# Performance work log

Hardware: AMD Instinct MI355X
Metric: run time of the kernel (lower is better)

## Reference

```python
import jax, jax.numpy as jnp
import numpy as np

D_MODEL = 1024
NUM_HEADS = 16
D_K = D_MODEL // NUM_HEADS


def setup_inputs() -> dict:
    key = jax.random.key(0)
    ks = jax.random.split(key, 7)
    B, S = 4, 2048
    scale = 1.0 / np.sqrt(D_MODEL)
    return {
        "query": jax.random.normal(ks[0], (B, S, D_MODEL), dtype=jnp.float32),
        "key": jax.random.normal(ks[1], (B, S, D_MODEL), dtype=jnp.float32),
        "value": jax.random.normal(ks[2], (B, S, D_MODEL), dtype=jnp.float32),
        "W_q": jax.random.normal(ks[3], (D_MODEL, D_MODEL), dtype=jnp.float32) * scale,
        "W_k": jax.random.normal(ks[4], (D_MODEL, D_MODEL), dtype=jnp.float32) * scale,
        "W_v": jax.random.normal(ks[5], (D_MODEL, D_MODEL), dtype=jnp.float32) * scale,
        "W_o": jax.random.normal(ks[6], (D_MODEL, D_MODEL), dtype=jnp.float32) * scale,
    }


def reference(query, key, value, W_q, W_k, W_v, W_o):
    B, S, _ = query.shape
    # nn.Linear applies x @ W.T; project then split heads: (B, H, S, d_k)
    def proj(x, W):
        return (x @ W.T).reshape(B, S, NUM_HEADS, D_K).transpose(0, 2, 1, 3)
    Q = proj(query, W_q)
    K = proj(key, W_k)
    V = proj(value, W_v)
    # naive full-score attention: (B, H, S, S)
    scores = jnp.einsum("bhqd,bhkd->bhqk", Q, K) / jnp.sqrt(jnp.float32(D_K))
    attn = jax.nn.softmax(scores, axis=-1)
    out = jnp.einsum("bhqk,bhkd->bhqd", attn, V)  # (B, H, S, d_k)
    out = out.transpose(0, 2, 1, 3).reshape(B, S, D_MODEL)
    return out @ W_o.T
```

## Files before the change

kernel.cpp:

```cpp
#include <hip/hip_runtime.h>
#include <hip/hip_bf16.h>
#include <cstdint>
#include <cstddef>

static constexpr int S  = 2048;
static constexpr int DM = 1024;
static constexpr int NH = 16;
static constexpr int BB = 4;
static constexpr int MR = BB * S;

typedef __bf16 bf16x8 __attribute__((ext_vector_type(8)));
typedef float  f32x4  __attribute__((ext_vector_type(4)));
typedef float  f32x16 __attribute__((ext_vector_type(16)));
typedef unsigned int uint2v __attribute__((ext_vector_type(2)));

__device__ __forceinline__ f32x4 mfma16(bf16x8 a, bf16x8 b, f32x4 c) {
    return __builtin_amdgcn_mfma_f32_16x16x32_bf16(a, b, c, 0, 0, 0);
}
__device__ __forceinline__ f32x16 mfma32(bf16x8 a, bf16x8 b, f32x16 c) {
    return __builtin_amdgcn_mfma_f32_32x32x16_bf16(a, b, c, 0, 0, 0);
}

__device__ __forceinline__ unsigned int cvt_pk_bf16(float lo, float hi) {
    unsigned int r;
    asm("v_cvt_pk_bf16_f32 %0, %1, %2" : "=v"(r) : "v"(lo), "v"(hi));
    return r;
}

struct CvtArgs {
    const float* src[7];
    __hip_bfloat16* dst[7];
    int n[7];
    float scl[7];
};

__global__ __launch_bounds__(256) void cvt_kernel(CvtArgs a) {
    const int t = blockIdx.y;
    const int i = (blockIdx.x * 256 + threadIdx.x) * 4;
    if (i >= a.n[t]) return;
    const float s = a.scl[t];
    const float4 v = *reinterpret_cast<const float4*>(a.src[t] + i);
    union { __hip_bfloat16 h[4]; short4 s4; } u;
    u.h[0] = __float2bfloat16(v.x * s);
    u.h[1] = __float2bfloat16(v.y * s);
    u.h[2] = __float2bfloat16(v.z * s);
    u.h[3] = __float2bfloat16(v.w * s);
    *reinterpret_cast<short4*>(a.dst[t] + i) = u.s4;
}

struct ProjArgs {
    const __hip_bfloat16* X[3];
    const __hip_bfloat16* W[3];
    __hip_bfloat16* O[3];
};

__global__ __launch_bounds__(256) void proj_kernel(ProjArgs a)
{
    __shared__ __align__(16) unsigned char smem[65536];
    __hip_bfloat16* Ts = reinterpret_cast<__hip_bfloat16*>(smem);

    const int id    = blockIdx.x;
    const int which = id >> 9;
    const int rem   = id & 511;
    const int xcd   = rem & 7, idx = rem >> 3;
    const int ystrip = xcd * 8 + (idx >> 3);
    const int xblk   = idx & 7;

    const __hip_bfloat16* __restrict__ X = a.X[which];
    const __hip_bfloat16* __restrict__ W = a.W[which];
    __hip_bfloat16* __restrict__ O = a.O[which];

    const int tid  = threadIdx.x;
    const int wave = tid >> 6, lane = tid & 63;
    const int wm = wave >> 1, wn = wave & 1;
    const int lr = lane & 15, lg = lane >> 4;
    const int m0 = ystrip * 128;
    const int n0 = xblk * 128;
    constexpr int K = DM;

    const int srow = tid >> 3, scol = (tid & 7) * 8;

    auto stage = [&](int bsel, int kt) {
        __hip_bfloat16* As = reinterpret_cast<__hip_bfloat16*>(smem + bsel * 32768);
        __hip_bfloat16* Bs = reinterpret_cast<__hip_bfloat16*>(smem + bsel * 32768 + 16384);
#pragma unroll
        for (int r = 0; r < 4; ++r) {
            const int c = r * 256 + tid;
            const int row = srow + r * 32;
            __builtin_amdgcn_global_load_lds(
                (const __attribute__((address_space(1))) void*)&X[(size_t)(m0 + row) * K + kt + scol],
                (__attribute__((address_space(3))) void*)&As[c * 8], 16, 0, 0);
            __builtin_amdgcn_global_load_lds(
                (const __attribute__((address_space(1))) void*)&W[(size_t)(n0 + row) * K + kt + scol],
                (__attribute__((address_space(3))) void*)&Bs[c * 8], 16, 0, 0);
        }
    };

    f32x4 acc[4][4] = {};

    stage(0, 0);
    int cur = 0;
    for (int kt = 0; kt < K; kt += 64) {
        __syncthreads();
        if (kt + 64 < K) stage(cur ^ 1, kt + 64);

        const __hip_bfloat16* As = reinterpret_cast<const __hip_bfloat16*>(smem + cur * 32768);
        const __hip_bfloat16* Bs = reinterpret_cast<const __hip_bfloat16*>(smem + cur * 32768 + 16384);
#pragma unroll
        for (int ks = 0; ks < 2; ++ks) {
            bf16x8 af[4], bfr[4];
#pragma unroll
            for (int i = 0; i < 4; ++i)
                af[i] = *reinterpret_cast<const bf16x8*>(&As[(wm * 64 + i * 16 + lr) * 64 + ks * 32 + lg * 8]);
#pragma unroll
            for (int i = 0; i < 4; ++i)
                bfr[i] = *reinterpret_cast<const bf16x8*>(&Bs[(wn * 64 + i * 16 + lr) * 64 + ks * 32 + lg * 8]);
#pragma unroll
            for (int mi = 0; mi < 4; ++mi)
#pragma unroll
                for (int ni = 0; ni < 4; ++ni)
                    acc[mi][ni] = mfma16(af[mi], bfr[ni], acc[mi][ni]);
        }
        cur ^= 1;
    }

    __syncthreads();
    if (which == 2) {
#pragma unroll
        for (int mi = 0; mi < 4; ++mi)
#pragma unroll
            for (int ni = 0; ni < 4; ++ni)
#pragma unroll
                for (int j = 0; j < 4; ++j) {
                    const int nl = wn * 64 + ni * 16 + lr;
                    const int ml = wm * 64 + mi * 16 + lg * 4 + j;
                    Ts[nl * 136 + ml] = __float2bfloat16(acc[mi][ni][j]);
                }
        __syncthreads();
        const int b = m0 >> 11, s0 = m0 & (S - 1);
#pragma unroll
        for (int r = 0; r < 8; ++r) {
            const int i2 = r * 256 + tid;
            const int nl = i2 >> 4, mc = i2 & 15;
            const uint4 val = *reinterpret_cast<const uint4*>(&Ts[nl * 136 + mc * 8]);
            const int h = (n0 + nl) >> 6, d = (n0 + nl) & 63;
            *reinterpret_cast<uint4*>(
                &O[(((size_t)b * NH + h) * 64 + d) * S + s0 + mc * 8]) = val;
        }
    } else {
#pragma unroll
        for (int mi = 0; mi < 4; ++mi)
#pragma unroll
            for (int ni = 0; ni < 4; ++ni)
#pragma unroll
                for (int j = 0; j < 4; ++j) {
                    const int ml = wm * 64 + mi * 16 + lg * 4 + j;
                    const int nl = wn * 64 + ni * 16 + lr;
                    Ts[ml * 136 + nl] = __float2bfloat16(acc[mi][ni][j]);
                }
        __syncthreads();
#pragma unroll
        for (int r = 0; r < 8; ++r) {
            const int i2 = r * 256 + tid;
            const int ml = i2 >> 4, mc = i2 & 15;
            const uint4 val = *reinterpret_cast<const uint4*>(&Ts[ml * 136 + mc * 8]);
            const int m = m0 + ml, n = n0 + mc * 8;
            const int b = m >> 11, s = m & (S - 1);
            const int h = n >> 6,  d = n & 63;
            *reinterpret_cast<uint4*>(
                &O[((((size_t)b * NH + h) * S + s) << 6) + d]) = val;
        }
    }
}

__global__ __launch_bounds__(256) void gemm_out(
    const __hip_bfloat16* __restrict__ X,
    const __hip_bfloat16* __restrict__ W,
    float* __restrict__ C, int M, int N, int K)
{
    __shared__ __align__(16) unsigned char smem[65536];

    const int id  = blockIdx.x;
    const int xcd = id & 7, idx = id >> 3;
    const int m0 = (xcd * 8 + (idx >> 3)) * 128;
    const int n0 = (idx & 7) * 128;

    const int tid  = threadIdx.x;
    const int wave = tid >> 6, lane = tid & 63;
    const int wm = wave >> 1, wn = wave & 1;
    const int lr = lane & 15, lg = lane >> 4;

    const int srow = tid >> 3, scol = (tid & 7) * 8;

    auto stage = [&](int bsel, int kt) {
        __hip_bfloat16* As = reinterpret_cast<__hip_bfloat16*>(smem + bsel * 32768);
        __hip_bfloat16* Bs = reinterpret_cast<__hip_bfloat16*>(smem + bsel * 32768 + 16384);
#pragma unroll
        for (int r = 0; r < 4; ++r) {
            const int c = r * 256 + tid;
            const int row = srow + r * 32;
            __builtin_amdgcn_global_load_lds(
                (const __attribute__((address_space(1))) void*)&X[(size_t)(m0 + row) * K + kt + scol],
                (__attribute__((address_space(3))) void*)&As[c * 8], 16, 0, 0);
            __builtin_amdgcn_global_load_lds(
                (const __attribute__((address_space(1))) void*)&W[(size_t)(n0 + row) * K + kt + scol],
                (__attribute__((address_space(3))) void*)&Bs[c * 8], 16, 0, 0);
        }
    };

    f32x4 acc[4][4] = {};

    stage(0, 0);
    int cur = 0;
    for (int kt = 0; kt < K; kt += 64) {
        __syncthreads();
        if (kt + 64 < K) stage(cur ^ 1, kt + 64);

        const __hip_bfloat16* As = reinterpret_cast<const __hip_bfloat16*>(smem + cur * 32768);
        const __hip_bfloat16* Bs = reinterpret_cast<const __hip_bfloat16*>(smem + cur * 32768 + 16384);
#pragma unroll
        for (int ks = 0; ks < 2; ++ks) {
            bf16x8 af[4], bfr[4];
#pragma unroll
            for (int i = 0; i < 4; ++i)
                af[i] = *reinterpret_cast<const bf16x8*>(&As[(wm * 64 + i * 16 + lr) * 64 + ks * 32 + lg * 8]);
#pragma unroll
            for (int i = 0; i < 4; ++i)
                bfr[i] = *reinterpret_cast<const bf16x8*>(&Bs[(wn * 64 + i * 16 + lr) * 64 + ks * 32 + lg * 8]);
#pragma unroll
            for (int mi = 0; mi < 4; ++mi)
#pragma unroll
                for (int ni = 0; ni < 4; ++ni)
                    acc[mi][ni] = mfma16(af[mi], bfr[ni], acc[mi][ni]);
        }
        cur ^= 1;
    }

#pragma unroll
    for (int mi = 0; mi < 4; ++mi)
#pragma unroll
        for (int ni = 0; ni < 4; ++ni)
#pragma unroll
            for (int j = 0; j < 4; ++j) {
                const int m = m0 + wm * 64 + mi * 16 + lg * 4 + j;
                const int n = n0 + wn * 64 + ni * 16 + lr;
                C[(size_t)m * N + n] = acc[mi][ni][j];
            }
}

__global__ __launch_bounds__(256) void attn_kernel(
    const __hip_bfloat16* __restrict__ Qp,
    const __hip_bfloat16* __restrict__ Kp,
    const __hip_bfloat16* __restrict__ VpT,
    __hip_bfloat16* __restrict__ Oc)
{
    constexpr int LP = 72;
    constexpr int NT = S / 64;
    __shared__ __hip_bfloat16 Ks[2][64][LP];
    __shared__ __hip_bfloat16 Vt[2][64][LP];

    const int tid  = threadIdx.x;
    const int wave = tid >> 6, lane = tid & 63;
    const int l31 = lane & 31, hi = lane >> 5;

    const int id  = blockIdx.x;
    const int xcd = id & 7, idx = id >> 3;
    const int bh   = xcd + 8 * (idx >> 4);
    const int qblk = idx & 15;

    const int b = bh >> 4, h = bh & (NH - 1);
    const int q0 = qblk * 128 + wave * 32;

    const __hip_bfloat16* Qh  = Qp  + (size_t)bh * S * 64;
    const __hip_bfloat16* Kh  = Kp  + (size_t)bh * S * 64;
    const __hip_bfloat16* VhT = VpT + (size_t)bh * S * 64;

    const int srow0 = tid >> 3,         scol = (tid & 7) * 8;
    const int srow1 = (256 + tid) >> 3;

    bf16x8 qf[4];
#pragma unroll
    for (int ds = 0; ds < 4; ++ds)
        qf[ds] = *reinterpret_cast<const bf16x8*>(
            &Qh[(size_t)(q0 + l31) * 64 + ds * 16 + hi * 8]);

    bf16x8 onesf;
#pragma unroll
    for (int i = 0; i < 8; ++i) onesf[i] = (__bf16)1.0f;

    f32x16 o[2] = {};
    f32x16 osum = {};
    const f32x16 zero16 = {};

    uint4 kreg0, kreg1, vreg0, vreg1;
    kreg0 = *reinterpret_cast<const uint4*>(&Kh[(size_t)srow0 * 64 + scol]);
    kreg1 = *reinterpret_cast<const uint4*>(&Kh[(size_t)srow1 * 64 + scol]);
    vreg0 = *reinterpret_cast<const uint4*>(&VhT[(size_t)srow0 * S + scol]);
    vreg1 = *reinterpret_cast<const uint4*>(&VhT[(size_t)srow1 * S + scol]);
    *reinterpret_cast<uint4*>(&Ks[0][srow0][scol]) = kreg0;
    *reinterpret_cast<uint4*>(&Ks[0][srow1][scol]) = kreg1;
    *reinterpret_cast<uint4*>(&Vt[0][srow0][scol]) = vreg0;
    *reinterpret_cast<uint4*>(&Vt[0][srow1][scol]) = vreg1;

    for (int t = 0; t < NT; ++t) {
        const int cur = t & 1;
        __syncthreads();

        if (t + 1 < NT) {
            const int kt = (t + 1) * 64;
            kreg0 = *reinterpret_cast<const uint4*>(&Kh[(size_t)(kt + srow0) * 64 + scol]);
            kreg1 = *reinterpret_cast<const uint4*>(&Kh[(size_t)(kt + srow1) * 64 + scol]);
            vreg0 = *reinterpret_cast<const uint4*>(&VhT[(size_t)srow0 * S + kt + scol]);
            vreg1 = *reinterpret_cast<const uint4*>(&VhT[(size_t)srow1 * S + kt + scol]);
        }

        f32x16 scf[2];
        __builtin_amdgcn_s_setprio(1);
        {
            bf16x8 kfr0 = *reinterpret_cast<const bf16x8*>(&Ks[cur][l31][hi * 8]);
            bf16x8 kfr1 = *reinterpret_cast<const bf16x8*>(&Ks[cur][32 + l31][hi * 8]);
            scf[0] = mfma32(kfr0, qf[0], zero16);
            scf[1] = mfma32(kfr1, qf[0], zero16);
        }
#pragma unroll
        for (int ds = 1; ds < 4; ++ds) {
            bf16x8 kfr0 = *reinterpret_cast<const bf16x8*>(&Ks[cur][l31][ds * 16 + hi * 8]);
            bf16x8 kfr1 = *reinterpret_cast<const bf16x8*>(&Ks[cur][32 + l31][ds * 16 + hi * 8]);
            scf[0] = mfma32(kfr0, qf[ds], scf[0]);
            scf[1] = mfma32(kfr1, qf[ds], scf[1]);
        }
        __builtin_amdgcn_s_setprio(0);

        unsigned int w[2][8];
#pragma unroll
        for (int kf = 0; kf < 2; ++kf)
#pragma unroll
            for (int t8 = 0; t8 < 8; ++t8)
                w[kf][t8] = cvt_pk_bf16(
                    __builtin_amdgcn_exp2f(scf[kf][2 * t8]),
                    __builtin_amdgcn_exp2f(scf[kf][2 * t8 + 1]));

        __builtin_amdgcn_s_setprio(1);
#pragma unroll
        for (int kb = 0; kb < 4; ++kb) {
            const int kf = kb >> 1, tb = (kb & 1) * 4;
            uint2v r02 = __builtin_amdgcn_permlane32_swap(w[kf][tb + 0], w[kf][tb + 2], false, false);
            uint2v r13 = __builtin_amdgcn_permlane32_swap(w[kf][tb + 1], w[kf][tb + 3], false, false);
            union { unsigned int u[4]; bf16x8 v; } pf;
            pf.u[0] = r02[0]; pf.u[1] = r13[0]; pf.u[2] = r02[1]; pf.u[3] = r13[1];
            bf16x8 vf0 = *reinterpret_cast<const bf16x8*>(&Vt[cur][l31][kb * 16 + hi * 8]);
            bf16x8 vf1 = *reinterpret_cast<const bf16x8*>(&Vt[cur][32 + l31][kb * 16 + hi * 8]);
            o[0] = mfma32(pf.v, vf0, o[0]);
            o[1] = mfma32(pf.v, vf1, o[1]);
            osum = mfma32(pf.v, onesf, osum);
        }
        __builtin_amdgcn_s_setprio(0);

        if (t + 1 < NT) {
            const int nxt = cur ^ 1;
            *reinterpret_cast<uint4*>(&Ks[nxt][srow0][scol]) = kreg0;
            *reinterpret_cast<uint4*>(&Ks[nxt][srow1][scol]) = kreg1;
            *reinterpret_cast<uint4*>(&Vt[nxt][srow0][scol]) = vreg0;
            *reinterpret_cast<uint4*>(&Vt[nxt][srow1][scol]) = vreg1;
        }
    }

    float inv[16];
#pragma unroll
    for (int r = 0; r < 16; ++r) inv[r] = 1.0f / osum[r];
#pragma unroll
    for (int df = 0; df < 2; ++df)
#pragma unroll
        for (int r = 0; r < 16; ++r) {
            const int qrow = (r & 3) + 8 * (r >> 2) + 4 * hi;
            const size_t row = (size_t)b * S + q0 + qrow;
            const int col = h * 64 + df * 32 + l31;
            Oc[row * DM + col] = __float2bfloat16(o[df][r] * inv[r]);
        }
}

extern "C" void kernel_launch(void* const* d_in, const int* in_sizes, int n_in,
                              void* d_out, int out_size, void* d_ws, size_t ws_size,
                              hipStream_t stream)
{
    const float* q  = (const float*)d_in[0];
    const float* k  = (const float*)d_in[1];
    const float* v  = (const float*)d_in[2];
    const float* wq = (const float*)d_in[3];
    const float* wk = (const float*)d_in[4];
    const float* wv = (const float*)d_in[5];
    const float* wo = (const float*)d_in[6];

    const size_t NE = (size_t)MR * DM;
    const size_t WE = (size_t)DM * DM;

    const size_t need = (7 * NE + 4 * WE) * sizeof(__hip_bfloat16);
    if (ws_size < need) return;

    __hip_bfloat16* p   = (__hip_bfloat16*)d_ws;
    __hip_bfloat16* qb  = p; p += NE;
    __hip_bfloat16* kb  = p; p += NE;
    __hip_bfloat16* vb  = p; p += NE;
    __hip_bfloat16* wqb = p; p += WE;
    __hip_bfloat16* wkb = p; p += WE;
    __hip_bfloat16* wvb = p; p += WE;
    __hip_bfloat16* wob = p; p += WE;
    __hip_bfloat16* Qp  = p; p += NE;
    __hip_bfloat16* Kp  = p; p += NE;
    __hip_bfloat16* VpT = p; p += NE;
    __hip_bfloat16* Oc  = p; p += NE;

    constexpr float SC = 0.18033688011112042f;

    CvtArgs ca;
    ca.src[0] = q;  ca.src[1] = k;  ca.src[2] = v;
    ca.src[3] = wq; ca.src[4] = wk; ca.src[5] = wv; ca.src[6] = wo;
    ca.dst[0] = qb;  ca.dst[1] = kb;  ca.dst[2] = vb;
    ca.dst[3] = wqb; ca.dst[4] = wkb; ca.dst[5] = wvb; ca.dst[6] = wob;
    for (int i = 0; i < 7; ++i) {
        ca.n[i] = (i < 3) ? (int)NE : (int)WE;
        ca.scl[i] = (i == 3) ? SC : 1.0f;
    }

    cvt_kernel<<<dim3((unsigned)(NE / 1024), 7), 256, 0, stream>>>(ca);

    ProjArgs pa;
    pa.X[0] = qb;  pa.X[1] = kb;  pa.X[2] = vb;
    pa.W[0] = wqb; pa.W[1] = wkb; pa.W[2] = wvb;
    pa.O[0] = Qp;  pa.O[1] = Kp;  pa.O[2] = VpT;

    proj_kernel<<<dim3(1536), 256, 0, stream>>>(pa);

    attn_kernel<<<dim3(1024), 256, 0, stream>>>(Qp, Kp, VpT, Oc);

    gemm_out<<<dim3(512), 256, 0, stream>>>(Oc, wob, (float*)d_out, MR, DM, DM);
}
```

Before: 207.2 us.

## Fuse fp32-to-bf16 activation conversion into projection GEMM A-tile loads

The projection kernel now reads fp32 query/key/value directly into registers, converts them to bf16 and writes them to LDS after the MFMA loop, prefetching the next tile. The standalone conversion pass over the three large activations is dropped, and the converter now handles only the four weight matrices. This removes a full read/write round trip of about 100MB of activation traffic and shrinks the workspace. The cost is twice the global read bytes per A tile inside the GEMM, plus extra registers and VALU conversion work that may reduce occupancy or overlap.

Result: no change. 210.6 us (+1.6%).

```diff
diff --git a/kernel.cpp b/kernel.cpp
--- a/kernel.cpp
+++ b/kernel.cpp
@@ -28,10 +28,10 @@
 }
 
 struct CvtArgs {
-    const float* src[7];
-    __hip_bfloat16* dst[7];
-    int n[7];
-    float scl[7];
+    const float* src[4];
+    __hip_bfloat16* dst[4];
+    int n[4];
+    float scl[4];
 };
 
 __global__ __launch_bounds__(256) void cvt_kernel(CvtArgs a) {
@@ -49,7 +49,7 @@
 }
 
 struct ProjArgs {
-    const __hip_bfloat16* X[3];
+    const float* X[3];
     const __hip_bfloat16* W[3];
     __hip_bfloat16* O[3];
 };
@@ -66,7 +66,7 @@
     const int ystrip = xcd * 8 + (idx >> 3);
     const int xblk   = idx & 7;
 
-    const __hip_bfloat16* __restrict__ X = a.X[which];
+    const float* __restrict__ X = a.X[which];
     const __hip_bfloat16* __restrict__ W = a.W[which];
     __hip_bfloat16* __restrict__ O = a.O[which];
 
@@ -80,29 +80,49 @@
 
     const int srow = tid >> 3, scol = (tid & 7) * 8;
 
-    auto stage = [&](int bsel, int kt) {
-        __hip_bfloat16* As = reinterpret_cast<__hip_bfloat16*>(smem + bsel * 32768);
+    float4 areg[8];
+
+    auto issue = [&](int bsel, int kt) {
         __hip_bfloat16* Bs = reinterpret_cast<__hip_bfloat16*>(smem + bsel * 32768 + 16384);
 #pragma unroll
         for (int r = 0; r < 4; ++r) {
             const int c = r * 256 + tid;
             const int row = srow + r * 32;
-            __builtin_amdgcn_global_load_lds(
-                (const __attribute__((address_space(1))) void*)&X[(size_t)(m0 + row) * K + kt + scol],
-                (__attribute__((address_space(3))) void*)&As[c * 8], 16, 0, 0);
+            const float* src = &X[(size_t)(m0 + row) * K + kt + scol];
+            areg[2 * r]     = *reinterpret_cast<const float4*>(src);
+            areg[2 * r + 1] = *reinterpret_cast<const float4*>(src + 4);
             __builtin_amdgcn_global_load_lds(
                 (const __attribute__((address_space(1))) void*)&W[(size_t)(n0 + row) * K + kt + scol],
                 (__attribute__((address_space(3))) void*)&Bs[c * 8], 16, 0, 0);
         }
     };
+    auto writeA = [&](int bsel) {
+        __hip_bfloat16* As = reinterpret_cast<__hip_bfloat16*>(smem + bsel * 32768);
+#pragma unroll
+        for (int r = 0; r < 4; ++r) {
+            const int c = r * 256 + tid;
+            union { __hip_bfloat16 h[8]; uint4 u4; } pk;
+            pk.h[0] = __float2bfloat16(areg[2 * r].x);
+            pk.h[1] = __float2bfloat16(areg[2 * r].y);
+            pk.h[2] = __float2bfloat16(areg[2 * r].z);
+            pk.h[3] = __float2bfloat16(areg[2 * r].w);
+            pk.h[4] = __float2bfloat16(areg[2 * r + 1].x);
+            pk.h[5] = __float2bfloat16(areg[2 * r + 1].y);
+            pk.h[6] = __float2bfloat16(areg[2 * r + 1].z);
+            pk.h[7] = __float2bfloat16(areg[2 * r + 1].w);
+            *reinterpret_cast<uint4*>(&As[c * 8]) = pk.u4;
+        }
+    };
 
     f32x4 acc[4][4] = {};
 
-    stage(0, 0);
+    issue(0, 0);
+    writeA(0);
     int cur = 0;
     for (int kt = 0; kt < K; kt += 64) {
         __syncthreads();
-        if (kt + 64 < K) stage(cur ^ 1, kt + 64);
+        const bool more = (kt + 64 < K);
+        if (more) issue(cur ^ 1, kt + 64);
 
         const __hip_bfloat16* As = reinterpret_cast<const __hip_bfloat16*>(smem + cur * 32768);
         const __hip_bfloat16* Bs = reinterpret_cast<const __hip_bfloat16*>(smem + cur * 32768 + 16384);
@@ -121,6 +141,7 @@
                 for (int ni = 0; ni < 4; ++ni)
                     acc[mi][ni] = mfma16(af[mi], bfr[ni], acc[mi][ni]);
         }
+        if (more) writeA(cur ^ 1);
         cur ^= 1;
     }
 
@@ -394,13 +415,10 @@
     const size_t NE = (size_t)MR * DM;
     const size_t WE = (size_t)DM * DM;
 
-    const size_t need = (7 * NE + 4 * WE) * sizeof(__hip_bfloat16);
+    const size_t need = (4 * NE + 4 * WE) * sizeof(__hip_bfloat16);
     if (ws_size < need) return;
 
     __hip_bfloat16* p   = (__hip_bfloat16*)d_ws;
-    __hip_bfloat16* qb  = p; p += NE;
-    __hip_bfloat16* kb  = p; p += NE;
-    __hip_bfloat16* vb  = p; p += NE;
     __hip_bfloat16* wqb = p; p += WE;
     __hip_bfloat16* wkb = p; p += WE;
     __hip_bfloat16* wvb = p; p += WE;
@@ -413,19 +431,17 @@
     constexpr float SC = 0.18033688011112042f;
 
     CvtArgs ca;
-    ca.src[0] = q;  ca.src[1] = k;  ca.src[2] = v;
-    ca.src[3] = wq; ca.src[4] = wk; ca.src[5] = wv; ca.src[6] = wo;
-    ca.dst[0] = qb;  ca.dst[1] = kb;  ca.dst[2] = vb;
-    ca.dst[3] = wqb; ca.dst[4] = wkb; ca.dst[5] = wvb; ca.dst[6] = wob;
-    for (int i = 0; i < 7; ++i) {
-        ca.n[i] = (i < 3) ? (int)NE : (int)WE;
-        ca.scl[i] = (i == 3) ? SC : 1.0f;
+    ca.src[0] = wq; ca.src[1] = wk; ca.src[2] = wv; ca.src[3] = wo;
+    ca.dst[0] = wqb; ca.dst[1] = wkb; ca.dst[2] = wvb; ca.dst[3] = wob;
+    for (int i = 0; i < 4; ++i) {
+        ca.n[i] = (int)WE;
+        ca.scl[i] = (i == 0) ? SC : 1.0f;
     }
 
-    cvt_kernel<<<dim3((unsigned)(NE / 1024), 7), 256, 0, stream>>>(ca);
+    cvt_kernel<<<dim3((unsigned)(WE / 1024), 4), 256, 0, stream>>>(ca);
 
     ProjArgs pa;
-    pa.X[0] = qb;  pa.X[1] = kb;  pa.X[2] = vb;
+    pa.X[0] = q;   pa.X[1] = k;   pa.X[2] = v;
     pa.W[0] = wqb; pa.W[1] = wkb; pa.W[2] = wvb;
     pa.O[0] = Qp;  pa.O[1] = Kp;  pa.O[2] = VpT;
 
```
